# Kernel optimization log

Measured on AMD Instinct MI355X. Metric: run time of the kernel, lower is better.

## Reference

```python
import jax, jax.numpy as jnp
import numpy as np

MULTI_INFER_NUM = 8
D_EMBED = 128
T, B = 256, 32


def setup_inputs() -> dict:
    key = jax.random.key(0)
    k1, k2, k3, k4 = jax.random.split(key, 4)
    positions = jax.random.randint(k1, (T, B), 0, 12, dtype=jnp.int64)
    outputs = jax.random.normal(k2, (T, B, D_EMBED), dtype=jnp.float32)
    W = jax.random.normal(k3, (MULTI_INFER_NUM + 1, D_EMBED, D_EMBED), dtype=jnp.float32)
    b = jax.random.normal(k4, (MULTI_INFER_NUM + 1, D_EMBED), dtype=jnp.float32)
    return {"positions": positions, "outputs": outputs, "W": W, "b": b}


def reference(positions, outputs, W, b):
    # Clamp positions >= multi_infer_num to the last (overflow) expert slot.
    r_pos = jnp.where(positions < MULTI_INFER_NUM, positions, MULTI_INFER_NUM)  # [T,B]
    # Gather per-token d x d transfer matrix, then batched matvec + bias,
    # matching tf.nn.embedding_lookup + einsum('ibde,ibd->ibe').
    w_gathered = W[r_pos]                         # [T,B,d,d]
    y = jnp.einsum('tbde,tbd->tbe', w_gathered, outputs)
    y = y + b[r_pos]                              # [T,B,d]
    return y
```

## Files before the change

### kernel.cpp

```cpp
#include <hip/hip_runtime.h>
#include <cstdint>

#define D 128
#define NEXP 9
#define TPB 256

__device__ __forceinline__ uint32_t pack2_bf16(float a, float b) {
    uint32_t ua = __builtin_bit_cast(uint32_t, a);
    uint32_t ub = __builtin_bit_cast(uint32_t, b);
    ua += 0x7fffu + ((ua >> 16) & 1u);
    ub += 0x7fffu + ((ub >> 16) & 1u);
    return (ua >> 16) | (ub & 0xffff0000u);
}

__global__ __launch_bounds__(TPB, 1) void ltf_kernel(
    const int* __restrict__ pos, const float* __restrict__ x,
    const float* __restrict__ W, const float* __restrict__ bias,
    float* __restrict__ y, int ntok, int c0)
{
    __shared__ uint32_t Wp[D * (D / 2)];
    __shared__ float XT[4][D * 8];
    __shared__ int lst[256];
    __shared__ int cnt;

    const int tid = threadIdx.x;
    const int lane = tid & 63;
    const int wv = tid >> 6;
    const int bid = blockIdx.x;

    int r, start, C;
    if (bid < 8 * c0) { r = bid / c0; start = (bid - r * c0) * 256; C = 256; }
    else              { r = 8; start = (bid - 8 * c0) * 64; C = 64; }

    if (tid == 0) cnt = 0;

    const float2* Wr2 = reinterpret_cast<const float2*>(W + (size_t)r * D * D);
    #pragma unroll
    for (int i = 0; i < (D * D / 2) / TPB; ++i) {
        int idx = i * TPB + tid;
        float2 w = Wr2[idx];
        Wp[idx] = pack2_bf16(w.x, w.y);
    }
    __syncthreads();

    if (wv < (C >> 6)) {
        int t = start + (wv << 6) + lane;
        bool m = false;
        if (t < ntok) {
            int p = pos[t];
            int rp = p < (NEXP - 1) ? p : (NEXP - 1);
            m = (rp == r);
        }
        unsigned long long mask = __ballot(m);
        int pre = __popcll(mask & ((1ull << lane) - 1ull));
        int nm = __popcll(mask);
        int base = 0;
        if (lane == 0 && nm > 0) base = atomicAdd(&cnt, nm);
        base = __shfl(base, 0);
        if (m) lst[base + pre] = t;
    }
    __syncthreads();

    const int nc = cnt;
    float* xt = XT[wv];
    const float2 bv = reinterpret_cast<const float2*>(bias + (size_t)r * D)[lane];

    for (int g = wv; g * 8 < nc; g += 4) {
        const int gb = g * 8;
        int valid = nc - gb; if (valid > 8) valid = 8;

        const int ti = lane >> 3, seg = lane & 7;
        int tsel = ti < valid ? ti : valid - 1;
        int mytok = lst[gb + tsel];
        const float4* xs = reinterpret_cast<const float4*>(x + (size_t)mytok * D + seg * 16);
        #pragma unroll
        for (int j = 0; j < 4; ++j) {
            float4 v = xs[j];
            int d0 = seg * 16 + j * 4;
            xt[(d0 + 0) * 8 + ti] = v.x;
            xt[(d0 + 1) * 8 + ti] = v.y;
            xt[(d0 + 2) * 8 + ti] = v.z;
            xt[(d0 + 3) * 8 + ti] = v.w;
        }

        float acc0[8], acc1[8];
        #pragma unroll
        for (int t = 0; t < 8; ++t) { acc0[t] = 0.f; acc1[t] = 0.f; }

        #pragma unroll 4
        for (int d = 0; d < D; ++d) {
            uint32_t w2 = Wp[d * 64 + lane];
            float w0 = __builtin_bit_cast(float, w2 << 16);
            float w1 = __builtin_bit_cast(float, w2 & 0xffff0000u);
            const float4* xr = reinterpret_cast<const float4*>(&xt[d * 8]);
            float4 a = xr[0];
            float4 c = xr[1];
            acc0[0] += w0 * a.x; acc1[0] += w1 * a.x;
            acc0[1] += w0 * a.y; acc1[1] += w1 * a.y;
            acc0[2] += w0 * a.z; acc1[2] += w1 * a.z;
            acc0[3] += w0 * a.w; acc1[3] += w1 * a.w;
            acc0[4] += w0 * c.x; acc1[4] += w1 * c.x;
            acc0[5] += w0 * c.y; acc1[5] += w1 * c.y;
            acc0[6] += w0 * c.z; acc1[6] += w1 * c.z;
            acc0[7] += w0 * c.w; acc1[7] += w1 * c.w;
        }

        #pragma unroll
        for (int t = 0; t < 8; ++t) {
            if (t < valid) {
                int tk = lst[gb + t];
                float2 o;
                o.x = acc0[t] + bv.x;
                o.y = acc1[t] + bv.y;
                reinterpret_cast<float2*>(y + (size_t)tk * D)[lane] = o;
            }
        }
    }
}

extern "C" void kernel_launch(void* const* d_in, const int* in_sizes, int n_in,
                              void* d_out, int out_size, void* d_ws, size_t ws_size,
                              hipStream_t stream) {
    const int* pos  = (const int*)d_in[0];
    const float* x  = (const float*)d_in[1];
    const float* W  = (const float*)d_in[2];
    const float* b  = (const float*)d_in[3];
    float* y = (float*)d_out;

    int ntok = in_sizes[0];
    int c0 = (ntok + 255) / 256;
    int grid = 8 * c0 + (ntok + 63) / 64;
    ltf_kernel<<<grid, TPB, 0, stream>>>(pos, x, W, b, y, ntok, c0);
}
```

Baseline: 75.51 us.

## Split into global per-expert compaction pass and tiled apply kernel over output halves

Adds a separate compaction kernel that buckets token indices per expert into a workspace via ballots and atomics. The apply kernel then launches one block per 64-token tile of each expert, split into two output-column halves, so each block loads only half of one expert's weights. This removes the old design where every block scanned all tokens to find its expert's matches, wasting most blocks on non-matching tokens. The cost is a memset, an extra kernel launch and a global index round trip, and some launched blocks exit early because the grid is sized for the worst case.

```diff
diff --git a/kernel.cpp b/kernel.cpp
--- a/kernel.cpp
+++ b/kernel.cpp
@@ -3,7 +3,6 @@
 
 #define D 128
 #define NEXP 9
-#define TPB 256
 
 __device__ __forceinline__ uint32_t pack2_bf16(float a, float b) {
     uint32_t ua = __builtin_bit_cast(uint32_t, a);
@@ -13,106 +12,137 @@
     return (ua >> 16) | (ub & 0xffff0000u);
 }
 
-__global__ __launch_bounds__(TPB, 1) void ltf_kernel(
-    const int* __restrict__ pos, const float* __restrict__ x,
-    const float* __restrict__ W, const float* __restrict__ bias,
-    float* __restrict__ y, int ntok, int c0)
+__global__ void ltf_compact(const int* __restrict__ pos, int ntok,
+                            int* __restrict__ cnt, int* __restrict__ idx)
 {
-    __shared__ uint32_t Wp[D * (D / 2)];
-    __shared__ float XT[4][D * 8];
-    __shared__ int lst[256];
-    __shared__ int cnt;
+    __shared__ int lcnt[NEXP];
+    __shared__ int gbase[NEXP];
+    const int tid = threadIdx.x;
+    const int lane = tid & 63;
+    const int t = blockIdx.x * 256 + tid;
+
+    if (tid < NEXP) lcnt[tid] = 0;
+    __syncthreads();
+
+    int rp = NEXP;
+    if (t < ntok) { int p = pos[t]; rp = p < NEXP - 1 ? p : NEXP - 1; }
+
+    unsigned long long m[NEXP];
+    #pragma unroll
+    for (int r = 0; r < NEXP; ++r) m[r] = __ballot(rp == r);
+
+    int wb = 0;
+    if (lane < NEXP) {
+        int cm = __popcll(m[lane]);
+        if (cm) wb = atomicAdd(&lcnt[lane], cm);
+    }
+    __syncthreads();
+    if (tid < NEXP) gbase[tid] = lcnt[tid] ? atomicAdd(&cnt[tid], lcnt[tid]) : 0;
+    __syncthreads();
+
+    if (t < ntok) {
+        int pre = __popcll(m[rp] & ((1ull << lane) - 1ull));
+        int slot = gbase[rp] + __shfl(wb, rp) + pre;
+        idx[rp * ntok + slot] = t;
+    }
+}
+
+__global__ __launch_bounds__(256) void ltf_apply(
+    const float* __restrict__ x, const float* __restrict__ W,
+    const float* __restrict__ bias, const int* __restrict__ cnt,
+    const int* __restrict__ idx, float* __restrict__ y, int ntok)
+{
+    __shared__ uint32_t Wp[D * 32];
+    __shared__ float XT[4][D * 16];
 
     const int tid = threadIdx.x;
     const int lane = tid & 63;
     const int wv = tid >> 6;
-    const int bid = blockIdx.x;
+    const int fid = blockIdx.x >> 1;
+    const int half = blockIdx.x & 1;
 
-    int r, start, C;
-    if (bid < 8 * c0) { r = bid / c0; start = (bid - r * c0) * 256; C = 256; }
-    else              { r = 8; start = (bid - 8 * c0) * 64; C = 64; }
+    int r = -1, tile = 0, acct = 0, cr = 0;
+    #pragma unroll
+    for (int i = 0; i < NEXP; ++i) {
+        int ci = cnt[i];
+        int tr = (ci + 63) >> 6;
+        if (r < 0 && fid < acct + tr) { r = i; tile = fid - acct; cr = ci; }
+        acct += tr;
+    }
+    if (r < 0) return;
 
-    if (tid == 0) cnt = 0;
+    const int base = tile * 64;
+    int nv = cr - base; if (nv > 64) nv = 64;
 
-    const float2* Wr2 = reinterpret_cast<const float2*>(W + (size_t)r * D * D);
+    const float* Wr = W + (size_t)r * D * D + half * 64;
     #pragma unroll
-    for (int i = 0; i < (D * D / 2) / TPB; ++i) {
-        int idx = i * TPB + tid;
-        float2 w = Wr2[idx];
-        Wp[idx] = pack2_bf16(w.x, w.y);
+    for (int i = 0; i < 16; ++i) {
+        int id = i * 256 + tid;
+        int d = id >> 5, ep = id & 31;
+        float2 w = *reinterpret_cast<const float2*>(Wr + d * D + ep * 2);
+        Wp[id] = pack2_bf16(w.x, w.y);
     }
-    __syncthreads();
 
-    if (wv < (C >> 6)) {
-        int t = start + (wv << 6) + lane;
-        bool m = false;
-        if (t < ntok) {
-            int p = pos[t];
-            int rp = p < (NEXP - 1) ? p : (NEXP - 1);
-            m = (rp == r);
-        }
-        unsigned long long mask = __ballot(m);
-        int pre = __popcll(mask & ((1ull << lane) - 1ull));
-        int nm = __popcll(mask);
-        int base = 0;
-        if (lane == 0 && nm > 0) base = atomicAdd(&cnt, nm);
-        base = __shfl(base, 0);
-        if (m) lst[base + pre] = t;
-    }
-    __syncthreads();
-
-    const int nc = cnt;
+    const int* lst = idx + r * ntok + base;
     float* xt = XT[wv];
-    const float2 bv = reinterpret_cast<const float2*>(bias + (size_t)r * D)[lane];
-
-    for (int g = wv; g * 8 < nc; g += 4) {
-        const int gb = g * 8;
-        int valid = nc - gb; if (valid > 8) valid = 8;
-
-        const int ti = lane >> 3, seg = lane & 7;
-        int tsel = ti < valid ? ti : valid - 1;
-        int mytok = lst[gb + tsel];
-        const float4* xs = reinterpret_cast<const float4*>(x + (size_t)mytok * D + seg * 16);
+    #pragma unroll
+    for (int p = 0; p < 2; ++p) {
+        int tloc = wv * 16 + p * 8 + (lane >> 3);
+        int tcl = tloc < nv ? tloc : nv - 1;
+        int tok = lst[tcl];
+        const int seg = lane & 7;
+        const float4* xs = reinterpret_cast<const float4*>(x + (size_t)tok * D + seg * 16);
         #pragma unroll
         for (int j = 0; j < 4; ++j) {
             float4 v = xs[j];
             int d0 = seg * 16 + j * 4;
-            xt[(d0 + 0) * 8 + ti] = v.x;
-            xt[(d0 + 1) * 8 + ti] = v.y;
-            xt[(d0 + 2) * 8 + ti] = v.z;
-            xt[(d0 + 3) * 8 + ti] = v.w;
+            int q = p * 8 + (lane >> 3);
+            xt[(d0 + 0) * 16 + q] = v.x;
+            xt[(d0 + 1) * 16 + q] = v.y;
+            xt[(d0 + 2) * 16 + q] = v.z;
+            xt[(d0 + 3) * 16 + q] = v.w;
         }
+    }
+    __syncthreads();
 
-        float acc0[8], acc1[8];
+    const int ep = lane & 31;
+    const int tsub = lane >> 5;
+    const float2 bv = *reinterpret_cast<const float2*>(
+        bias + (size_t)r * D + half * 64 + ep * 2);
+
+    int nw = nv - wv * 16; if (nw > 16) nw = 16;
+    if (nw > 0) {
+        float a0[8], a1[8];
         #pragma unroll
-        for (int t = 0; t < 8; ++t) { acc0[t] = 0.f; acc1[t] = 0.f; }
+        for (int t = 0; t < 8; ++t) { a0[t] = 0.f; a1[t] = 0.f; }
 
-        #pragma unroll 4
+        #pragma unroll 8
         for (int d = 0; d < D; ++d) {
-            uint32_t w2 = Wp[d * 64 + lane];
+            uint32_t w2 = Wp[d * 32 + ep];
             float w0 = __builtin_bit_cast(float, w2 << 16);
             float w1 = __builtin_bit_cast(float, w2 & 0xffff0000u);
-            const float4* xr = reinterpret_cast<const float4*>(&xt[d * 8]);
-            float4 a = xr[0];
-            float4 c = xr[1];
-            acc0[0] += w0 * a.x; acc1[0] += w1 * a.x;
-            acc0[1] += w0 * a.y; acc1[1] += w1 * a.y;
-            acc0[2] += w0 * a.z; acc1[2] += w1 * a.z;
-            acc0[3] += w0 * a.w; acc1[3] += w1 * a.w;
-            acc0[4] += w0 * c.x; acc1[4] += w1 * c.x;
-            acc0[5] += w0 * c.y; acc1[5] += w1 * c.y;
-            acc0[6] += w0 * c.z; acc1[6] += w1 * c.z;
-            acc0[7] += w0 * c.w; acc1[7] += w1 * c.w;
+            const float4* xr = reinterpret_cast<const float4*>(&xt[d * 16 + tsub * 8]);
+            float4 va = xr[0];
+            float4 vb = xr[1];
+            a0[0] += w0 * va.x; a1[0] += w1 * va.x;
+            a0[1] += w0 * va.y; a1[1] += w1 * va.y;
+            a0[2] += w0 * va.z; a1[2] += w1 * va.z;
+            a0[3] += w0 * va.w; a1[3] += w1 * va.w;
+            a0[4] += w0 * vb.x; a1[4] += w1 * vb.x;
+            a0[5] += w0 * vb.y; a1[5] += w1 * vb.y;
+            a0[6] += w0 * vb.z; a1[6] += w1 * vb.z;
+            a0[7] += w0 * vb.w; a1[7] += w1 * vb.w;
         }
 
         #pragma unroll
         for (int t = 0; t < 8; ++t) {
-            if (t < valid) {
-                int tk = lst[gb + t];
+            int tloc = wv * 16 + tsub * 8 + t;
+            if (tloc < nv) {
+                int tok = lst[tloc];
                 float2 o;
-                o.x = acc0[t] + bv.x;
-                o.y = acc1[t] + bv.y;
-                reinterpret_cast<float2*>(y + (size_t)tk * D)[lane] = o;
+                o.x = a0[t] + bv.x;
+                o.y = a1[t] + bv.y;
+                reinterpret_cast<float2*>(y + (size_t)tok * D + half * 64)[ep] = o;
             }
         }
     }
@@ -127,8 +157,13 @@
     const float* b  = (const float*)d_in[3];
     float* y = (float*)d_out;
 
-    int ntok = in_sizes[0];
-    int c0 = (ntok + 255) / 256;
-    int grid = 8 * c0 + (ntok + 63) / 64;
-    ltf_kernel<<<grid, TPB, 0, stream>>>(pos, x, W, b, y, ntok, c0);
+    const int ntok = in_sizes[0];
+    int* cnt = (int*)d_ws;
+    int* idx = cnt + 16;
+
+    hipMemsetAsync(d_ws, 0, 64, stream);
+    ltf_compact<<<(ntok + 255) / 256, 256, 0, stream>>>(pos, ntok, cnt, idx);
+
+    int nblk = 2 * ((ntok + 63) / 64 + NEXP);
+    ltf_apply<<<nblk, 256, 0, stream>>>(x, W, b, cnt, idx, y, ntok);
 }
```

Result: slower. 78.73 us (+4.3%).

## Double per-block token chunk, overlap position scan with weight staging

Applied to the files above, without the earlier changes.

Each block now scans 512 tokens for experts 0-7 (128 for the overflow expert) instead of 256/64, so there are half as many blocks and each staged bf16 copy of the weight matrix is reused across more tokens. The position scan now runs before the weight load, so its global reads can overlap the weight fetch. Weight staging uses float4 loads, and the launch-bounds occupancy hint is relaxed. The trade-off is fewer blocks to spread across the GPU and more sequential token groups per wave.

```diff
diff --git a/kernel.cpp b/kernel.cpp
--- a/kernel.cpp
+++ b/kernel.cpp
@@ -4,6 +4,8 @@
 #define D 128
 #define NEXP 9
 #define TPB 256
+#define CH0 512
+#define CH8 128
 
 __device__ __forceinline__ uint32_t pack2_bf16(float a, float b) {
     uint32_t ua = __builtin_bit_cast(uint32_t, a);
@@ -13,14 +15,14 @@
     return (ua >> 16) | (ub & 0xffff0000u);
 }
 
-__global__ __launch_bounds__(TPB, 1) void ltf_kernel(
+__global__ __launch_bounds__(TPB) void ltf_kernel(
     const int* __restrict__ pos, const float* __restrict__ x,
     const float* __restrict__ W, const float* __restrict__ bias,
     float* __restrict__ y, int ntok, int c0)
 {
     __shared__ uint32_t Wp[D * (D / 2)];
     __shared__ float XT[4][D * 8];
-    __shared__ int lst[256];
+    __shared__ int lst[CH0];
     __shared__ int cnt;
 
     const int tid = threadIdx.x;
@@ -29,35 +31,40 @@
     const int bid = blockIdx.x;
 
     int r, start, C;
-    if (bid < 8 * c0) { r = bid / c0; start = (bid - r * c0) * 256; C = 256; }
-    else              { r = 8; start = (bid - 8 * c0) * 64; C = 64; }
+    if (bid < 8 * c0) { r = bid / c0; start = (bid - r * c0) * CH0; C = CH0; }
+    else              { r = 8; start = (bid - 8 * c0) * CH8; C = CH8; }
 
     if (tid == 0) cnt = 0;
-
-    const float2* Wr2 = reinterpret_cast<const float2*>(W + (size_t)r * D * D);
-    #pragma unroll
-    for (int i = 0; i < (D * D / 2) / TPB; ++i) {
-        int idx = i * TPB + tid;
-        float2 w = Wr2[idx];
-        Wp[idx] = pack2_bf16(w.x, w.y);
-    }
     __syncthreads();
 
-    if (wv < (C >> 6)) {
-        int t = start + (wv << 6) + lane;
+    const int end = (start + C < ntok) ? start + C : ntok;
+    #pragma unroll
+    for (int it = 0; it < CH0 / TPB; ++it) {
+        int t = start + it * TPB + tid;
         bool m = false;
-        if (t < ntok) {
+        if (t < end) {
             int p = pos[t];
             int rp = p < (NEXP - 1) ? p : (NEXP - 1);
             m = (rp == r);
         }
         unsigned long long mask = __ballot(m);
-        int pre = __popcll(mask & ((1ull << lane) - 1ull));
         int nm = __popcll(mask);
         int base = 0;
         if (lane == 0 && nm > 0) base = atomicAdd(&cnt, nm);
         base = __shfl(base, 0);
-        if (m) lst[base + pre] = t;
+        if (m) {
+            int pre = __popcll(mask & ((1ull << lane) - 1ull));
+            lst[base + pre] = t;
+        }
+    }
+
+    const float4* Wr4 = reinterpret_cast<const float4*>(W + (size_t)r * D * D);
+    #pragma unroll
+    for (int i = 0; i < (D * D / 4) / TPB; ++i) {
+        int idx = i * TPB + tid;
+        float4 w = Wr4[idx];
+        Wp[idx * 2 + 0] = pack2_bf16(w.x, w.y);
+        Wp[idx * 2 + 1] = pack2_bf16(w.z, w.w);
     }
     __syncthreads();
 
@@ -83,9 +90,9 @@
             xt[(d0 + 3) * 8 + ti] = v.w;
         }
 
-        float acc0[8], acc1[8];
+        float a0[8], a1[8];
         #pragma unroll
-        for (int t = 0; t < 8; ++t) { acc0[t] = 0.f; acc1[t] = 0.f; }
+        for (int t = 0; t < 8; ++t) { a0[t] = 0.f; a1[t] = 0.f; }
 
         #pragma unroll 4
         for (int d = 0; d < D; ++d) {
@@ -93,16 +100,16 @@
             float w0 = __builtin_bit_cast(float, w2 << 16);
             float w1 = __builtin_bit_cast(float, w2 & 0xffff0000u);
             const float4* xr = reinterpret_cast<const float4*>(&xt[d * 8]);
-            float4 a = xr[0];
-            float4 c = xr[1];
-            acc0[0] += w0 * a.x; acc1[0] += w1 * a.x;
-            acc0[1] += w0 * a.y; acc1[1] += w1 * a.y;
-            acc0[2] += w0 * a.z; acc1[2] += w1 * a.z;
-            acc0[3] += w0 * a.w; acc1[3] += w1 * a.w;
-            acc0[4] += w0 * c.x; acc1[4] += w1 * c.x;
-            acc0[5] += w0 * c.y; acc1[5] += w1 * c.y;
-            acc0[6] += w0 * c.z; acc1[6] += w1 * c.z;
-            acc0[7] += w0 * c.w; acc1[7] += w1 * c.w;
+            float4 va = xr[0];
+            float4 vb = xr[1];
+            a0[0] += w0 * va.x; a1[0] += w1 * va.x;
+            a0[1] += w0 * va.y; a1[1] += w1 * va.y;
+            a0[2] += w0 * va.z; a1[2] += w1 * va.z;
+            a0[3] += w0 * va.w; a1[3] += w1 * va.w;
+            a0[4] += w0 * vb.x; a1[4] += w1 * vb.x;
+            a0[5] += w0 * vb.y; a1[5] += w1 * vb.y;
+            a0[6] += w0 * vb.z; a1[6] += w1 * vb.z;
+            a0[7] += w0 * vb.w; a1[7] += w1 * vb.w;
         }
 
         #pragma unroll
@@ -110,8 +117,8 @@
             if (t < valid) {
                 int tk = lst[gb + t];
                 float2 o;
-                o.x = acc0[t] + bv.x;
-                o.y = acc1[t] + bv.y;
+                o.x = a0[t] + bv.x;
+                o.y = a1[t] + bv.y;
                 reinterpret_cast<float2*>(y + (size_t)tk * D)[lane] = o;
             }
         }
@@ -127,8 +134,8 @@
     const float* b  = (const float*)d_in[3];
     float* y = (float*)d_out;
 
-    int ntok = in_sizes[0];
-    int c0 = (ntok + 255) / 256;
-    int grid = 8 * c0 + (ntok + 63) / 64;
-    ltf_kernel<<<grid, TPB, 0, stream>>>(pos, x, W, b, y, ntok, c0);
+    const int ntok = in_sizes[0];
+    const int c0 = (ntok + CH0 - 1) / CH0;
+    const int c8 = (ntok + CH8 - 1) / CH8;
+    ltf_kernel<<<8 * c0 + c8, TPB, 0, stream>>>(pos, x, W, b, y, ntok, c0);
 }
```

Result: no change. 76.72 us (+1.6%).
